# Kernel optimization log

Hardware: AMD Instinct MI355X
Metric: run time of the kernel (lower is better)

## Reference

```python
import jax, jax.numpy as jnp
import numpy as np

N = 50000      # nodes
E = 600000     # edges
F_IN = 11      # QM9 node features
H = 128        # hidden_channels
L = 5          # num_layers
G = 2048       # number of graphs in batch
EPS = 1e-5


def setup_inputs() -> dict:
    key = jax.random.key(0)
    ks = jax.random.split(key, 12)
    x = jax.random.normal(ks[0], (N, F_IN), dtype=jnp.float32)
    edge_index = jax.random.randint(ks[1], (2, E), 0, N, dtype=jnp.int64)
    batch = jnp.sort(jax.random.randint(ks[2], (N,), 0, G, dtype=jnp.int64))
    W0 = jax.random.normal(ks[3], (F_IN, H), dtype=jnp.float32) * 0.1
    b0 = jnp.zeros((H,), jnp.float32)
    Ws = jax.random.normal(ks[4], (L - 1, H, H), dtype=jnp.float32) * 0.05
    bs = jnp.zeros((L - 1, H), jnp.float32)
    bn_gamma = jnp.ones((L, H), jnp.float32)
    bn_beta = jnp.zeros((L, H), jnp.float32)
    bn_mean = jax.random.normal(ks[5], (L, H), dtype=jnp.float32) * 0.1
    bn_var = jax.random.uniform(ks[6], (L, H), minval=0.5, maxval=1.5, dtype=jnp.float32)
    lin1_w = jax.random.normal(ks[7], (H, H // 2), dtype=jnp.float32) * 0.05
    lin1_b = jnp.zeros((H // 2,), jnp.float32)
    lin2_w = jax.random.normal(ks[8], (H // 2, 1), dtype=jnp.float32) * 0.1
    lin2_b = jnp.zeros((1,), jnp.float32)
    return {"x": x, "edge_index": edge_index, "batch": batch,
            "W0": W0, "b0": b0, "Ws": Ws, "bs": bs,
            "bn_gamma": bn_gamma, "bn_beta": bn_beta,
            "bn_mean": bn_mean, "bn_var": bn_var,
            "lin1_w": lin1_w, "lin1_b": lin1_b,
            "lin2_w": lin2_w, "lin2_b": lin2_b}


def reference(x, edge_index, batch, W0, b0, Ws, bs, bn_gamma, bn_beta,
              bn_mean, bn_var, lin1_w, lin1_b, lin2_w, lin2_b):
    n = x.shape[0]
    # --- add self-loops (PyG GCNConv default) ---
    loop = jnp.arange(n, dtype=edge_index.dtype)
    src = jnp.concatenate([edge_index[0], loop])
    dst = jnp.concatenate([edge_index[1], loop])
    # symmetric normalization: deg over dst including self-loops (>=1)
    deg = jax.ops.segment_sum(jnp.ones(src.shape[0], x.dtype), dst, num_segments=n)
    dinv = jax.lax.rsqrt(deg)
    norm = (dinv[src] * dinv[dst])[:, None]  # [E+N, 1]

    for i in range(L):
        W = W0 if i == 0 else Ws[i - 1]
        b = b0 if i == 0 else bs[i - 1]
        h = x @ W                                            # [N, H]
        agg = jax.ops.segment_sum(h[src] * norm, dst, num_segments=n) + b
        # BatchNorm (eval mode: running stats) + ReLU
        xb = (agg - bn_mean[i]) * jax.lax.rsqrt(bn_var[i] + EPS) * bn_gamma[i] + bn_beta[i]
        xn = jax.nn.relu(xb)
        # residual only when shapes match and i > 0
        x = x + xn if (i > 0 and x.shape[-1] == xn.shape[-1]) else xn

    # --- global mean pool over graph ids ---
    sums = jax.ops.segment_sum(x, batch, num_segments=G)          # [G, H]
    cnts = jax.ops.segment_sum(jnp.ones((n,), x.dtype), batch, num_segments=G)
    pooled = sums / jnp.maximum(cnts, 1.0)[:, None]
    # dropout is identity in inference
    h1 = jax.nn.relu(pooled @ lin1_w + lin1_b)
    out = h1 @ lin2_w + lin2_b                                    # [G, 1]
    return out
```

## Files before the change

### kernel.cpp

```cpp
#include <hip/hip_runtime.h>
#include <hip/hip_fp16.h>

#define HDIM 128
#define BN_EPS 1e-5f

typedef _Float16 f16x8 __attribute__((ext_vector_type(8)));
typedef _Float16 f16x4 __attribute__((ext_vector_type(4)));
typedef float    f32x4 __attribute__((ext_vector_type(4)));

__device__ inline float4 ld_h4(const _Float16* p) {
    f16x4 r = *(const f16x4*)p;
    return make_float4((float)r.x, (float)r.y, (float)r.z, (float)r.w);
}

__device__ inline void st_h4(_Float16* p, float4 v) {
    f16x4 o = { (_Float16)v.x, (_Float16)v.y, (_Float16)v.z, (_Float16)v.w };
    *(f16x4*)p = o;
}


__global__ void k_zero2(int* __restrict__ a, int* __restrict__ b, int n) {
    int i = blockIdx.x * blockDim.x + threadIdx.x;
    if (i < n) { a[i] = 0; b[i] = 0; }
}

__global__ void k_deg_accum(const int* __restrict__ dst, int* __restrict__ deg, int e) {
    int i = blockIdx.x * blockDim.x + threadIdx.x;
    if (i < e) atomicAdd(&deg[dst[i]], 1);
}

__global__ void k_dinv(const int* __restrict__ deg, float* __restrict__ dinv, int n) {
    int i = blockIdx.x * blockDim.x + threadIdx.x;
    if (i < n) dinv[i] = rsqrtf((float)deg[i] + 1.0f);
}

__global__ void k_scan1(const int* __restrict__ deg, int* __restrict__ rs,
                        int* __restrict__ blk, int n) {
    __shared__ int s[256];
    int i = blockIdx.x * 256 + threadIdx.x;
    int v = (i < n) ? deg[i] : 0;
    s[threadIdx.x] = v;
    __syncthreads();
    for (int off = 1; off < 256; off <<= 1) {
        int t = (threadIdx.x >= off) ? s[threadIdx.x - off] : 0;
        __syncthreads();
        s[threadIdx.x] += t;
        __syncthreads();
    }
    if (i < n) rs[i] = s[threadIdx.x] - v;
    if (threadIdx.x == 255) blk[blockIdx.x] = s[255];
}

__global__ void k_scan2(int* __restrict__ blk, int nb) {
    __shared__ int s[256];
    int t = threadIdx.x;
    int v = (t < nb) ? blk[t] : 0;
    s[t] = v;
    __syncthreads();
    for (int off = 1; off < 256; off <<= 1) {
        int u = (t >= off) ? s[t - off] : 0;
        __syncthreads();
        s[t] += u;
        __syncthreads();
    }
    if (t < nb) blk[t] = s[t] - v;
}

__global__ void k_scan3(int* __restrict__ rs, const int* __restrict__ blk, int n) {
    int i = blockIdx.x * 256 + threadIdx.x;
    if (i < n) rs[i] += blk[blockIdx.x];
}

__global__ void k_fill(const int* __restrict__ src, const int* __restrict__ dst,
                       const int* __restrict__ rs, int* __restrict__ cur,
                       int* __restrict__ csr, int e) {
    int i = blockIdx.x * blockDim.x + threadIdx.x;
    if (i >= e) return;
    int d = dst[i];
    int pos = rs[d] + atomicAdd(&cur[d], 1);
    csr[pos] = src[i];
}

__global__ void k_bounds(const int* __restrict__ batch, int* __restrict__ bnd,
                         int n, int g) {
    int i = blockIdx.x * blockDim.x + threadIdx.x;
    if (i >= n) return;
    int b = batch[i];
    if (i == 0) {
        for (int q = 0; q <= b; ++q) bnd[q] = 0;
    } else {
        int p = batch[i - 1];
        for (int q = p + 1; q <= b; ++q) bnd[q] = i;
    }
    if (i == n - 1) {
        for (int q = b + 1; q <= g; ++q) bnd[q] = n;
    }
}

__global__ __launch_bounds__(256) void k_wconv_all(const float* __restrict__ Ws,
                                                   _Float16* __restrict__ wt, int nmats) {
    int idx = blockIdx.x * 256 + threadIdx.x;
    if (idx >= nmats * HDIM * HDIM) return;
    int l = idx >> 14, rem = idx & 16383;
    int k = rem >> 7, c = rem & 127;
    wt[(size_t)l * HDIM * HDIM + (size_t)c * HDIM + k] =
        (_Float16)Ws[(size_t)l * HDIM * HDIM + (size_t)k * HDIM + c];
}

__global__ __launch_bounds__(256) void k_gemm0(
    const float* __restrict__ x, const float* __restrict__ W,
    const float* __restrict__ dinv, _Float16* __restrict__ hs, int n, int fin) {
    int row = blockIdx.x * 2 + (threadIdx.x >> 7);
    int f = threadIdx.x & 127;
    if (row >= n) return;
    float acc = 0.0f;
    for (int k = 0; k < fin; ++k)
        acc += x[row * fin + k] * W[k * HDIM + f];
    hs[(size_t)row * HDIM + f] = (_Float16)(acc * dinv[row]);
}

__global__ __launch_bounds__(256) void k_gemm_mfma(
    const _Float16* __restrict__ xh, const _Float16* __restrict__ wt,
    const float* __restrict__ dinv, _Float16* __restrict__ hs, int n) {
    int wid  = threadIdx.x >> 6;
    int lane = threadIdx.x & 63;
    int xr   = blockIdx.x * 64 + wid * 16 + (lane & 15);
    int kc   = (lane >> 4) * 8;

    f32x4 acc[8];
    #pragma unroll
    for (int t = 0; t < 8; ++t) acc[t] = (f32x4){0.f, 0.f, 0.f, 0.f};

    #pragma unroll
    for (int kb = 0; kb < HDIM; kb += 32) {
        f16x8 bfrag = {};
        if (xr < n) bfrag = *(const f16x8*)(xh + (size_t)xr * HDIM + kb + kc);
        #pragma unroll
        for (int t = 0; t < 8; ++t) {
            f16x8 afrag = *(const f16x8*)(wt + (size_t)(t * 16 + (lane & 15)) * HDIM + kb + kc);
            acc[t] = __builtin_amdgcn_mfma_f32_16x16x32_f16(afrag, bfrag, acc[t], 0, 0, 0);
        }
    }

    if (xr >= n) return;
    float di = dinv[xr];
    #pragma unroll
    for (int t = 0; t < 8; ++t) {
        int c0 = t * 16 + (lane >> 4) * 4;
        f16x4 o = { (_Float16)(acc[t][0] * di), (_Float16)(acc[t][1] * di),
                    (_Float16)(acc[t][2] * di), (_Float16)(acc[t][3] * di) };
        *(f16x4*)(hs + (size_t)xr * HDIM + c0) = o;
    }
}

__global__ __launch_bounds__(256) void k_agg(
    const int* __restrict__ rs, const int* __restrict__ deg,
    const int* __restrict__ csr, const _Float16* __restrict__ hs,
    const float* __restrict__ dinv, const float* __restrict__ bias,
    const float* __restrict__ gamma, const float* __restrict__ beta,
    const float* __restrict__ mean, const float* __restrict__ var,
    const float* __restrict__ xold, float* __restrict__ xnew,
    _Float16* __restrict__ xh, int n, int use_res) {
    int node = blockIdx.x * 8 + (threadIdx.x >> 5);
    if (node >= n) return;
    int f4 = (threadIdx.x & 31) * 4;
    size_t base = (size_t)node * HDIM + f4;

    float4 a0 = ld_h4(hs + base);
    float4 a1 = make_float4(0.f, 0.f, 0.f, 0.f);
    float4 a2 = make_float4(0.f, 0.f, 0.f, 0.f);
    float4 a3 = make_float4(0.f, 0.f, 0.f, 0.f);
    int start = rs[node];
    int d = deg[node];
    int j = 0;
    for (; j + 4 <= d; j += 4) {
        int s0 = csr[start + j];
        int s1 = csr[start + j + 1];
        int s2 = csr[start + j + 2];
        int s3 = csr[start + j + 3];
        float4 v0 = ld_h4(hs + (size_t)s0 * HDIM + f4);
        float4 v1 = ld_h4(hs + (size_t)s1 * HDIM + f4);
        float4 v2 = ld_h4(hs + (size_t)s2 * HDIM + f4);
        float4 v3 = ld_h4(hs + (size_t)s3 * HDIM + f4);
        a0.x += v0.x; a0.y += v0.y; a0.z += v0.z; a0.w += v0.w;
        a1.x += v1.x; a1.y += v1.y; a1.z += v1.z; a1.w += v1.w;
        a2.x += v2.x; a2.y += v2.y; a2.z += v2.z; a2.w += v2.w;
        a3.x += v3.x; a3.y += v3.y; a3.z += v3.z; a3.w += v3.w;
    }
    for (; j < d; ++j) {
        int s0 = csr[start + j];
        float4 v0 = ld_h4(hs + (size_t)s0 * HDIM + f4);
        a0.x += v0.x; a0.y += v0.y; a0.z += v0.z; a0.w += v0.w;
    }
    float4 acc;
    acc.x = (a0.x + a1.x) + (a2.x + a3.x);
    acc.y = (a0.y + a1.y) + (a2.y + a3.y);
    acc.z = (a0.z + a1.z) + (a2.z + a3.z);
    acc.w = (a0.w + a1.w) + (a2.w + a3.w);

    float di = dinv[node];
    float4 bv = *(const float4*)(bias + f4);
    float4 gv = *(const float4*)(gamma + f4);
    float4 be = *(const float4*)(beta + f4);
    float4 mv = *(const float4*)(mean + f4);
    float4 vv = *(const float4*)(var + f4);
    float4 o;
    o.x = fmaxf((di * acc.x + bv.x - mv.x) * rsqrtf(vv.x + BN_EPS) * gv.x + be.x, 0.f);
    o.y = fmaxf((di * acc.y + bv.y - mv.y) * rsqrtf(vv.y + BN_EPS) * gv.y + be.y, 0.f);
    o.z = fmaxf((di * acc.z + bv.z - mv.z) * rsqrtf(vv.z + BN_EPS) * gv.z + be.z, 0.f);
    o.w = fmaxf((di * acc.w + bv.w - mv.w) * rsqrtf(vv.w + BN_EPS) * gv.w + be.w, 0.f);
    if (use_res) {
        float4 xo = *(const float4*)(xold + base);
        o.x += xo.x; o.y += xo.y; o.z += xo.z; o.w += xo.w;
    }
    *(float4*)(xnew + base) = o;
    st_h4(xh + base, o);
}

__global__ __launch_bounds__(256) void k_pool_seg(
    const float* __restrict__ x, const int* __restrict__ bnd,
    float* __restrict__ pooled, int g) {
    int gid = blockIdx.x * 8 + (threadIdx.x >> 5);
    if (gid >= g) return;
    int f4 = (threadIdx.x & 31) * 4;
    int s = bnd[gid], t = bnd[gid + 1];
    float4 a0 = make_float4(0.f, 0.f, 0.f, 0.f);
    float4 a1 = make_float4(0.f, 0.f, 0.f, 0.f);
    int r = s;
    for (; r + 2 <= t; r += 2) {
        float4 v0 = *(const float4*)(x + (size_t)r * HDIM + f4);
        float4 v1 = *(const float4*)(x + (size_t)(r + 1) * HDIM + f4);
        a0.x += v0.x; a0.y += v0.y; a0.z += v0.z; a0.w += v0.w;
        a1.x += v1.x; a1.y += v1.y; a1.z += v1.z; a1.w += v1.w;
    }
    if (r < t) {
        float4 v0 = *(const float4*)(x + (size_t)r * HDIM + f4);
        a0.x += v0.x; a0.y += v0.y; a0.z += v0.z; a0.w += v0.w;
    }
    float inv = (t > s) ? 1.0f / (float)(t - s) : 0.0f;
    float4 o = make_float4((a0.x + a1.x) * inv, (a0.y + a1.y) * inv,
                           (a0.z + a1.z) * inv, (a0.w + a1.w) * inv);
    *(float4*)(pooled + (size_t)gid * HDIM + f4) = o;
}

__global__ __launch_bounds__(64) void k_head(
    const float* __restrict__ pooled,
    const float* __restrict__ w1, const float* __restrict__ b1,
    const float* __restrict__ w2, const float* __restrict__ b2,
    float* __restrict__ out) {
    __shared__ float p[HDIM];
    int g = blockIdx.x;
    int t = threadIdx.x;
    p[t]      = pooled[(size_t)g * HDIM + t];
    p[t + 64] = pooled[(size_t)g * HDIM + 64 + t];
    __syncthreads();
    float h = b1[t];
    #pragma unroll 4
    for (int k = 0; k < HDIM; ++k)
        h += p[k] * w1[k * 64 + t];
    h = fmaxf(h, 0.f);
    float part = h * w2[t];
    #pragma unroll
    for (int off = 32; off > 0; off >>= 1)
        part += __shfl_down(part, off);
    if (t == 0) out[g] = part + b2[0];
}

extern "C" void kernel_launch(void* const* d_in, const int* in_sizes, int n_in,
                              void* d_out, int out_size, void* d_ws, size_t ws_size,
                              hipStream_t stream) {
    const float* x0   = (const float*)d_in[0];
    const int*   eidx = (const int*)  d_in[1];
    const int*   batch= (const int*)  d_in[2];
    const float* W0   = (const float*)d_in[3];
    const float* b0   = (const float*)d_in[4];
    const float* Ws   = (const float*)d_in[5];
    const float* bs   = (const float*)d_in[6];
    const float* gam  = (const float*)d_in[7];
    const float* bet  = (const float*)d_in[8];
    const float* mean = (const float*)d_in[9];
    const float* var  = (const float*)d_in[10];
    const float* w1   = (const float*)d_in[11];
    const float* b1   = (const float*)d_in[12];
    const float* w2   = (const float*)d_in[13];
    const float* b2   = (const float*)d_in[14];

    const int FIN = 11;
    int n = in_sizes[0] / FIN;
    int e = in_sizes[1] / 2;
    int g = out_size;
    int nb = (n + 255) / 256;

    const int* src = eidx;
    const int* dst = eidx + e;

    char* ws = (char*)d_ws;
    size_t nal = ((size_t)n + 255) & ~(size_t)255;
    int*      deg   = (int*)ws;                    ws += nal * 4;
    int*      cur   = (int*)ws;                    ws += nal * 4;
    int*      rs    = (int*)ws;                    ws += nal * 4;
    int*      blk   = (int*)ws;                    ws += 256 * 4;
    int*      bnd   = (int*)ws;                    ws += ((size_t)g + 64) / 64 * 64 * 4;
    int*      csr   = (int*)ws;                    ws += ((size_t)e + 63) / 64 * 64 * 4;
    float*    dinv  = (float*)ws;                  ws += nal * 4;
    _Float16* wt    = (_Float16*)ws;               ws += (size_t)4 * HDIM * HDIM * 2;
    float*    bufA  = (float*)ws;                  ws += (size_t)n * HDIM * 4;
    _Float16* bufH  = (_Float16*)ws;               ws += (size_t)n * HDIM * 2;
    _Float16* xh    = (_Float16*)ws;               ws += (size_t)n * HDIM * 2;
    float*    pooled= (float*)ws;

    k_zero2<<<nb, 256, 0, stream>>>(deg, cur, n);
    k_deg_accum<<<(e + 255) / 256, 256, 0, stream>>>(dst, deg, e);
    k_dinv<<<nb, 256, 0, stream>>>(deg, dinv, n);
    k_scan1<<<nb, 256, 0, stream>>>(deg, rs, blk, n);
    k_scan2<<<1, 256, 0, stream>>>(blk, nb);
    k_scan3<<<nb, 256, 0, stream>>>(rs, blk, n);
    k_fill<<<(e + 255) / 256, 256, 0, stream>>>(src, dst, rs, cur, csr, e);
    k_bounds<<<nb, 256, 0, stream>>>(batch, bnd, n, g);
    k_wconv_all<<<(4 * HDIM * HDIM + 255) / 256, 256, 0, stream>>>(Ws, wt, 4);

    for (int i = 0; i < 5; ++i) {
        const float* xin = (i == 0) ? x0 : bufA;
        const float* bias = (i == 0) ? b0 : bs + (size_t)(i - 1) * HDIM;
        if (i == 0) {
            k_gemm0<<<(n + 1) / 2, 256, 0, stream>>>(x0, W0, dinv, bufH, n, FIN);
        } else {
            k_gemm_mfma<<<(n + 63) / 64, 256, 0, stream>>>(
                xh, wt + (size_t)(i - 1) * HDIM * HDIM, dinv, bufH, n);
        }
        k_agg<<<(n + 7) / 8, 256, 0, stream>>>(
            rs, deg, csr, bufH, dinv, bias,
            gam + i * HDIM, bet + i * HDIM, mean + i * HDIM, var + i * HDIM,
            xin, bufA, xh, n, (i > 0) ? 1 : 0);
    }

    k_pool_seg<<<(g + 7) / 8, 256, 0, stream>>>(bufA, bnd, pooled, g);
    k_head<<<g, 64, 0, stream>>>(pooled, w1, b1, w2, b2, (float*)d_out);
}
```

Measured before the change: 480.2 us.

## Store fp16 hidden features in 16-column slices to localize aggregation gathers

```diff
diff --git a/kernel.cpp b/kernel.cpp
--- a/kernel.cpp
+++ b/kernel.cpp
@@ -7,6 +7,7 @@
 typedef _Float16 f16x8 __attribute__((ext_vector_type(8)));
 typedef _Float16 f16x4 __attribute__((ext_vector_type(4)));
 typedef float    f32x4 __attribute__((ext_vector_type(4)));
+
 
 __device__ inline float4 ld_h4(const _Float16* p) {
     f16x4 r = *(const f16x4*)p;
@@ -116,7 +117,9 @@
     float acc = 0.0f;
     for (int k = 0; k < fin; ++k)
         acc += x[row * fin + k] * W[k * HDIM + f];
-    hs[(size_t)row * HDIM + f] = (_Float16)(acc * dinv[row]);
+    size_t n16 = (size_t)n * 16;
+    hs[(size_t)(f >> 4) * n16 + (size_t)row * 16 + (f & 15)] =
+        (_Float16)(acc * dinv[row]);
 }
 
 __global__ __launch_bounds__(256) void k_gemm_mfma(
@@ -126,6 +129,7 @@
     int lane = threadIdx.x & 63;
     int xr   = blockIdx.x * 64 + wid * 16 + (lane & 15);
     int kc   = (lane >> 4) * 8;
+    size_t n16 = (size_t)n * 16;
 
     f32x4 acc[8];
     #pragma unroll
@@ -133,8 +137,11 @@
 
     #pragma unroll
     for (int kb = 0; kb < HDIM; kb += 32) {
+        int f0 = kb + kc;
         f16x8 bfrag = {};
-        if (xr < n) bfrag = *(const f16x8*)(xh + (size_t)xr * HDIM + kb + kc);
+        if (xr < n)
+            bfrag = *(const f16x8*)(xh + (size_t)(f0 >> 4) * n16 +
+                                    (size_t)xr * 16 + (f0 & 15));
         #pragma unroll
         for (int t = 0; t < 8; ++t) {
             f16x8 afrag = *(const f16x8*)(wt + (size_t)(t * 16 + (lane & 15)) * HDIM + kb + kc);
@@ -146,10 +153,10 @@
     float di = dinv[xr];
     #pragma unroll
     for (int t = 0; t < 8; ++t) {
-        int c0 = t * 16 + (lane >> 4) * 4;
+        int w = (lane >> 4) * 4;
         f16x4 o = { (_Float16)(acc[t][0] * di), (_Float16)(acc[t][1] * di),
                     (_Float16)(acc[t][2] * di), (_Float16)(acc[t][3] * di) };
-        *(f16x4*)(hs + (size_t)xr * HDIM + c0) = o;
+        *(f16x4*)(hs + (size_t)t * n16 + (size_t)xr * 16 + w) = o;
     }
 }
 
@@ -161,12 +168,15 @@
     const float* __restrict__ mean, const float* __restrict__ var,
     const float* __restrict__ xold, float* __restrict__ xnew,
     _Float16* __restrict__ xh, int n, int use_res) {
-    int node = blockIdx.x * 8 + (threadIdx.x >> 5);
+    int slice = blockIdx.x & 7;
+    int node  = (blockIdx.x >> 3) * 64 + (threadIdx.x >> 2);
     if (node >= n) return;
-    int f4 = (threadIdx.x & 31) * 4;
-    size_t base = (size_t)node * HDIM + f4;
-
-    float4 a0 = ld_h4(hs + base);
+    int w = (threadIdx.x & 3) * 4;
+    int f = slice * 16 + w;
+    size_t n16 = (size_t)n * 16;
+    const _Float16* hss = hs + (size_t)slice * n16;
+
+    float4 a0 = ld_h4(hss + (size_t)node * 16 + w);
     float4 a1 = make_float4(0.f, 0.f, 0.f, 0.f);
     float4 a2 = make_float4(0.f, 0.f, 0.f, 0.f);
     float4 a3 = make_float4(0.f, 0.f, 0.f, 0.f);
@@ -178,10 +188,10 @@
         int s1 = csr[start + j + 1];
         int s2 = csr[start + j + 2];
         int s3 = csr[start + j + 3];
-        float4 v0 = ld_h4(hs + (size_t)s0 * HDIM + f4);
-        float4 v1 = ld_h4(hs + (size_t)s1 * HDIM + f4);
-        float4 v2 = ld_h4(hs + (size_t)s2 * HDIM + f4);
-        float4 v3 = ld_h4(hs + (size_t)s3 * HDIM + f4);
+        float4 v0 = ld_h4(hss + (size_t)s0 * 16 + w);
+        float4 v1 = ld_h4(hss + (size_t)s1 * 16 + w);
+        float4 v2 = ld_h4(hss + (size_t)s2 * 16 + w);
+        float4 v3 = ld_h4(hss + (size_t)s3 * 16 + w);
         a0.x += v0.x; a0.y += v0.y; a0.z += v0.z; a0.w += v0.w;
         a1.x += v1.x; a1.y += v1.y; a1.z += v1.z; a1.w += v1.w;
         a2.x += v2.x; a2.y += v2.y; a2.z += v2.z; a2.w += v2.w;
@@ -189,7 +199,7 @@
     }
     for (; j < d; ++j) {
         int s0 = csr[start + j];
-        float4 v0 = ld_h4(hs + (size_t)s0 * HDIM + f4);
+        float4 v0 = ld_h4(hss + (size_t)s0 * 16 + w);
         a0.x += v0.x; a0.y += v0.y; a0.z += v0.z; a0.w += v0.w;
     }
     float4 acc;
@@ -199,22 +209,23 @@
     acc.w = (a0.w + a1.w) + (a2.w + a3.w);
 
     float di = dinv[node];
-    float4 bv = *(const float4*)(bias + f4);
-    float4 gv = *(const float4*)(gamma + f4);
-    float4 be = *(const float4*)(beta + f4);
-    float4 mv = *(const float4*)(mean + f4);
-    float4 vv = *(const float4*)(var + f4);
+    float4 bv = *(const float4*)(bias + f);
+    float4 gv = *(const float4*)(gamma + f);
+    float4 be = *(const float4*)(beta + f);
+    float4 mv = *(const float4*)(mean + f);
+    float4 vv = *(const float4*)(var + f);
+    size_t rbase = (size_t)node * HDIM + f;
     float4 o;
     o.x = fmaxf((di * acc.x + bv.x - mv.x) * rsqrtf(vv.x + BN_EPS) * gv.x + be.x, 0.f);
     o.y = fmaxf((di * acc.y + bv.y - mv.y) * rsqrtf(vv.y + BN_EPS) * gv.y + be.y, 0.f);
     o.z = fmaxf((di * acc.z + bv.z - mv.z) * rsqrtf(vv.z + BN_EPS) * gv.z + be.z, 0.f);
     o.w = fmaxf((di * acc.w + bv.w - mv.w) * rsqrtf(vv.w + BN_EPS) * gv.w + be.w, 0.f);
     if (use_res) {
-        float4 xo = *(const float4*)(xold + base);
+        float4 xo = *(const float4*)(xold + rbase);
         o.x += xo.x; o.y += xo.y; o.z += xo.z; o.w += xo.w;
     }
-    *(float4*)(xnew + base) = o;
-    st_h4(xh + base, o);
+    *(float4*)(xnew + rbase) = o;
+    st_h4(xh + (size_t)slice * n16 + (size_t)node * 16 + w, o);
 }
 
 __global__ __launch_bounds__(256) void k_pool_seg(
@@ -319,6 +330,8 @@
     k_bounds<<<nb, 256, 0, stream>>>(batch, bnd, n, g);
     k_wconv_all<<<(4 * HDIM * HDIM + 255) / 256, 256, 0, stream>>>(Ws, wt, 4);
 
+    int aggGrid = ((n + 63) / 64) * 8;
+
     for (int i = 0; i < 5; ++i) {
         const float* xin = (i == 0) ? x0 : bufA;
         const float* bias = (i == 0) ? b0 : bs + (size_t)(i - 1) * HDIM;
@@ -328,7 +341,7 @@
             k_gemm_mfma<<<(n + 63) / 64, 256, 0, stream>>>(
                 xh, wt + (size_t)(i - 1) * HDIM * HDIM, dinv, bufH, n);
         }
-        k_agg<<<(n + 7) / 8, 256, 0, stream>>>(
+        k_agg<<<aggGrid, 256, 0, stream>>>(
             rs, deg, csr, bufH, dinv, bias,
             gam + i * HDIM, bet + i * HDIM, mean + i * HDIM, var + i * HDIM,
             xin, bufA, xh, n, (i > 0) ? 1 : 0);
```

After: 498.2 us. +3.7%, slower.
